# Performance work log

Hardware: AMD Instinct MI355X
Metric: run time of the kernel (lower is better)

The kernel has to match this reference:

```python
import jax, jax.numpy as jnp
import numpy as np

SCALE = 1.0

def setup_inputs() -> dict:
    key = jax.random.key(0)
    ks = jax.random.split(key, 7)
    B, S, I, O, R = 4, 4096, 1024, 1024, 256
    return {
        "x": jax.random.normal(ks[0], (B, S, I), dtype=jnp.float32),
        "base_weight": jax.random.normal(ks[1], (3 * O, I), dtype=jnp.float32) * 0.02,
        "base_bias": jax.random.normal(ks[2], (3 * O,), dtype=jnp.float32) * 0.02,
        "vera_A": jax.random.normal(ks[3], (R, I), dtype=jnp.float32) * 0.02,
        "vera_B": jax.random.normal(ks[4], (O, R), dtype=jnp.float32) * 0.02,
        "vera_d": jax.random.normal(ks[5], (2, R), dtype=jnp.float32) * 0.1,
        "vera_b": jax.random.normal(ks[6], (2, O), dtype=jnp.float32) * 0.1,
    }

def reference(x, base_weight, base_bias, vera_A, vera_B, vera_d, vera_b):
    # delta[k] = scale * diag(vera_b[k]) @ B @ diag(vera_d[k]) @ A  for k in {K, V}
    # implemented as (b[:,None]*B) @ (d[:,None]*A), batched over k via einsum
    O, I = vera_B.shape[0], vera_A.shape[1]
    deltas = SCALE * jnp.einsum("ko,or,kr,ri->koi", vera_b, vera_B, vera_d, vera_A)
    delta = deltas.reshape(2 * O, I)  # (2*O, I) stacked K,V deltas
    # kv_only=True: Q rows get zero delta, then K,V deltas
    zeros = jnp.zeros((base_weight.shape[0] - 2 * O, I), dtype=base_weight.dtype)
    full_delta = jnp.concatenate([zeros, delta], axis=0)  # (3*O, I)
    weight = base_weight + full_delta
    # linear: x @ weight.T + bias -> (B, S, 3*O)
    return jnp.einsum("bsi,oi->bso", x, weight) + base_bias
```

## Files before the change

### kernel.cpp

```cpp
#include <hip/hip_runtime.h>
#include <hip/hip_bf16.h>
#include <cstdint>
#include <cstddef>

typedef __bf16 bf16_t;
typedef __bf16 bf16x8 __attribute__((ext_vector_type(8)));
typedef __bf16 bf16x4 __attribute__((ext_vector_type(4)));
typedef float  f32x4  __attribute__((ext_vector_type(4)));

#define M_DIM 16384
#define N_DIM 3072
#define K_DIM 1024
#define R_DIM 256
#define O_DIM 1024

#define BM 128
#define BN 128
#define BK 32
#define NT_TILES 24
#define GRID_GEMM 3072
#define CHUNK_XCD 384

__device__ __forceinline__ void gload_lds16(const bf16_t* g, bf16_t* l) {
  __builtin_amdgcn_global_load_lds(
      (__attribute__((address_space(1))) void*)(g),
      (__attribute__((address_space(3))) void*)(l), 16, 0, 0);
}

__global__ __launch_bounds__(256) void prep_all(
    const float* __restrict__ x,
    const float* __restrict__ base_w,
    const float* __restrict__ vA,
    const float* __restrict__ vB,
    const float* __restrict__ vd,
    const float* __restrict__ vb,
    bf16_t* __restrict__ Wf,
    bf16_t* __restrict__ xh)
{
  const int blk = blockIdx.x;
  const int t = threadIdx.x;

  if (blk >= 384) {
    const size_t base = ((size_t)(blk - 384) * 256 + t) * 8;
    const f32x4 v0 = *(const f32x4*)(x + base);
    const f32x4 v1 = *(const f32x4*)(x + base + 4);
    bf16x8 o;
    o[0] = (bf16_t)v0[0]; o[1] = (bf16_t)v0[1]; o[2] = (bf16_t)v0[2]; o[3] = (bf16_t)v0[3];
    o[4] = (bf16_t)v1[0]; o[5] = (bf16_t)v1[1]; o[6] = (bf16_t)v1[2]; o[7] = (bf16_t)v1[3];
    *(bf16x8*)(xh + base) = o;
    return;
  }

  if (blk < 128) {
    const float* src = base_w + (size_t)blk * 8 * K_DIM;
    bf16_t*      dst = Wf + (size_t)blk * 8 * K_DIM;
#pragma unroll
    for (int rr = 0; rr < 8; ++rr) {
      const f32x4 v = *(const f32x4*)(src + rr * K_DIM + t * 4);
      bf16x4 ov;
      ov[0] = (bf16_t)v[0]; ov[1] = (bf16_t)v[1];
      ov[2] = (bf16_t)v[2]; ov[3] = (bf16_t)v[3];
      *(bf16x4*)(dst + rr * K_DIM + t * 4) = ov;
    }
    return;
  }

  const int rb = (blk - 128) * 8;
  const int k  = rb >> 10;
  const int ob = rb & 1023;

  __shared__ float coeffT[R_DIM][8];
  {
    const int r = t;
    const float d = vd[k * R_DIM + r];
#pragma unroll
    for (int rr = 0; rr < 8; ++rr) {
      const int o = ob + rr;
      coeffT[r][rr] = vb[k * O_DIM + o] * vB[(size_t)o * R_DIM + r] * d;
    }
  }
  __syncthreads();

  float acc[8][4];
#pragma unroll
  for (int rr = 0; rr < 8; ++rr)
#pragma unroll
    for (int c = 0; c < 4; ++c) acc[rr][c] = 0.0f;

  for (int r = 0; r < R_DIM; ++r) {
    const f32x4 av = *(const f32x4*)(vA + (size_t)r * K_DIM + t * 4);
    const f32x4 c0 = *(const f32x4*)&coeffT[r][0];
    const f32x4 c1 = *(const f32x4*)&coeffT[r][4];
#pragma unroll
    for (int rr = 0; rr < 8; ++rr) {
      const float cc = (rr < 4) ? c0[rr] : c1[rr - 4];
      acc[rr][0] += cc * av[0];
      acc[rr][1] += cc * av[1];
      acc[rr][2] += cc * av[2];
      acc[rr][3] += cc * av[3];
    }
  }

#pragma unroll
  for (int rr = 0; rr < 8; ++rr) {
    const size_t row = (size_t)(1024 + rb + rr);
    const f32x4 bw = *(const f32x4*)(base_w + row * K_DIM + t * 4);
    bf16x4 ov;
    ov[0] = (bf16_t)(bw[0] + acc[rr][0]);
    ov[1] = (bf16_t)(bw[1] + acc[rr][1]);
    ov[2] = (bf16_t)(bw[2] + acc[rr][2]);
    ov[3] = (bf16_t)(bw[3] + acc[rr][3]);
    *(bf16x4*)(Wf + row * K_DIM + t * 4) = ov;
  }
}

template <bool PRECONV>
__global__ __launch_bounds__(256) void gemm_qkv(
    const bf16_t* __restrict__ Xh,
    const float*  __restrict__ Xf,
    const bf16_t* __restrict__ W,
    const float*  __restrict__ bias,
    float* __restrict__ out)
{
  __shared__ bf16_t As[BM * BK];
  __shared__ bf16_t Bs[BN * BK];

  const int rawbid = blockIdx.x;
  const int bid = (rawbid & 7) * CHUNK_XCD + (rawbid >> 3);
  const int nt = bid % NT_TILES;
  const int mt = bid / NT_TILES;
  const int m0 = mt * BM;
  const int n0 = nt * BN;

  const int t = threadIdx.x;
  const int lane = t & 63;
  const int w = t >> 6;
  const int wm = w >> 1;
  const int wn = w & 1;

  const int r0 = t >> 2;
  const int c0 = (t & 3) * 8;

  const bf16_t* gB0 = W + (size_t)(n0 + r0) * K_DIM + c0;
  const bf16_t* gB1 = gB0 + (size_t)64 * K_DIM;
  bf16_t* lA0 = As + r0 * BK + c0;
  bf16_t* lA1 = As + (r0 + 64) * BK + c0;
  bf16_t* lB0 = Bs + r0 * BK + c0;
  bf16_t* lB1 = Bs + (r0 + 64) * BK + c0;

  const bf16_t* gA0h = nullptr; const bf16_t* gA1h = nullptr;
  const float*  gA0f = nullptr; const float*  gA1f = nullptr;
  if constexpr (PRECONV) {
    gA0h = Xh + (size_t)(m0 + r0) * K_DIM + c0;
    gA1h = gA0h + (size_t)64 * K_DIM;
  } else {
    gA0f = Xf + (size_t)(m0 + r0) * K_DIM + c0;
    gA1f = gA0f + (size_t)64 * K_DIM;
  }

  const f32x4 zero4 = {0.0f, 0.0f, 0.0f, 0.0f};
  f32x4 acc[4][4];
#pragma unroll
  for (int i = 0; i < 4; ++i)
#pragma unroll
    for (int j = 0; j < 4; ++j) acc[i][j] = zero4;

  const int row_a = wm * 64 + (lane & 15);
  const int row_b = wn * 64 + (lane & 15);
  const int kb = (lane >> 4) * 8;

  for (int k0 = 0; k0 < K_DIM; k0 += BK) {
    if constexpr (PRECONV) {
      gload_lds16(gA0h + k0, lA0);
      gload_lds16(gA1h + k0, lA1);
    } else {
      const f32x4 u0 = *(const f32x4*)(gA0f + k0);
      const f32x4 u1 = *(const f32x4*)(gA0f + k0 + 4);
      const f32x4 u2 = *(const f32x4*)(gA1f + k0);
      const f32x4 u3 = *(const f32x4*)(gA1f + k0 + 4);
      bf16x8 a0, a1;
#pragma unroll
      for (int c = 0; c < 4; ++c) {
        a0[c] = (bf16_t)u0[c]; a0[c + 4] = (bf16_t)u1[c];
        a1[c] = (bf16_t)u2[c]; a1[c + 4] = (bf16_t)u3[c];
      }
      *(bf16x8*)lA0 = a0;
      *(bf16x8*)lA1 = a1;
    }
    gload_lds16(gB0 + k0, lB0);
    gload_lds16(gB1 + k0, lB1);
    __syncthreads();

    bf16x8 a[4], b[4];
#pragma unroll
    for (int i = 0; i < 4; ++i)
      a[i] = *(const bf16x8*)(As + (row_a + i * 16) * BK + kb);
#pragma unroll
    for (int j = 0; j < 4; ++j)
      b[j] = *(const bf16x8*)(Bs + (row_b + j * 16) * BK + kb);

#pragma unroll
    for (int i = 0; i < 4; ++i)
#pragma unroll
      for (int j = 0; j < 4; ++j)
        acc[i][j] = __builtin_amdgcn_mfma_f32_16x16x32_bf16(a[i], b[j], acc[i][j], 0, 0, 0);

    __syncthreads();
  }

  const int colg = lane & 15;
  const int rq = (lane >> 4) * 4;
#pragma unroll
  for (int j = 0; j < 4; ++j) {
    const int n = n0 + wn * 64 + j * 16 + colg;
    const float bv = bias[n];
#pragma unroll
    for (int i = 0; i < 4; ++i) {
      const size_t mb = (size_t)(m0 + wm * 64 + i * 16 + rq);
#pragma unroll
      for (int r = 0; r < 4; ++r)
        out[(mb + r) * N_DIM + n] = acc[i][j][r] + bv;
    }
  }
}

extern "C" void kernel_launch(void* const* d_in, const int* in_sizes, int n_in,
                              void* d_out, int out_size, void* d_ws, size_t ws_size,
                              hipStream_t stream) {
  const float* x      = (const float*)d_in[0];
  const float* base_w = (const float*)d_in[1];
  const float* base_b = (const float*)d_in[2];
  const float* vA     = (const float*)d_in[3];
  const float* vB     = (const float*)d_in[4];
  const float* vd     = (const float*)d_in[5];
  const float* vb     = (const float*)d_in[6];
  float* out = (float*)d_out;

  const size_t xh_off   = 8u * 1024 * 1024;
  const size_t xh_bytes = (size_t)M_DIM * K_DIM * sizeof(bf16_t);

  bf16_t* Wf = (bf16_t*)d_ws;
  const bool preconv = ws_size >= xh_off + xh_bytes;
  bf16_t* Xh = preconv ? (bf16_t*)((char*)d_ws + xh_off) : nullptr;

  prep_all<<<preconv ? 8576 : 384, 256, 0, stream>>>(x, base_w, vA, vB, vd, vb, Wf, Xh);

  if (preconv)
    gemm_qkv<true><<<GRID_GEMM, 256, 0, stream>>>(Xh, nullptr, Wf, base_b, out);
  else
    gemm_qkv<false><<<GRID_GEMM, 256, 0, stream>>>(nullptr, x, Wf, base_b, out);
}
```

Measured before the change: 422.0 us.

## Add 256x256 double-buffered GEMM with swizzled LDS and interleaved prefetch

After: 412.0 us. 1.02x faster.

```diff
diff --git a/kernel.cpp b/kernel.cpp
--- a/kernel.cpp
+++ b/kernel.cpp
@@ -14,12 +14,15 @@
 #define R_DIM 256
 #define O_DIM 1024
 
-#define BM 128
-#define BN 128
-#define BK 32
-#define NT_TILES 24
-#define GRID_GEMM 3072
-#define CHUNK_XCD 384
+#define BM 256
+#define BN 256
+#define BK 64
+#define NTILE (N_DIM / BN)
+#define GRID_GEMM ((M_DIM / BM) * NTILE)
+#define CHUNK_XCD (GRID_GEMM / 8)
+#define SMEM_BYTES 131072
+
+#define REGN(c, isB, kh) ((c) * 32768 + (isB) * 16384 + (kh) * 8192)
 
 __device__ __forceinline__ void gload_lds16(const bf16_t* g, bf16_t* l) {
   __builtin_amdgcn_global_load_lds(
@@ -114,23 +117,169 @@
   }
 }
 
+__global__ __launch_bounds__(512, 2) void gemm_qkv(
+    const bf16_t* __restrict__ Xh,
+    const bf16_t* __restrict__ W,
+    const float*  __restrict__ bias,
+    float* __restrict__ out)
+{
+  extern __shared__ __align__(16) bf16_t sm[];
+
+  const int rawbid = blockIdx.x;
+  const int bid = (rawbid & 7) * CHUNK_XCD + (rawbid >> 3);
+  const int mt = bid / NTILE, nt = bid % NTILE;
+  const int m0 = mt * BM, n0 = nt * BN;
+
+  const int t = threadIdx.x;
+  const int lane = t & 63;
+  const int w = t >> 6;
+  const int wm = w >> 2;
+  const int wn = w & 3;
+
+  const int srow = t >> 2;
+  const int sig  = (t & 3) ^ ((t >> 3) & 3);
+  const bf16_t* pA0 = Xh + (size_t)(m0 + srow) * K_DIM + sig * 8;
+  const bf16_t* pA1 = pA0 + (size_t)128 * K_DIM;
+  const bf16_t* pB0 = W  + (size_t)(n0 + srow) * K_DIM + sig * 8;
+  const bf16_t* pB1 = pB0 + (size_t)128 * K_DIM;
+
+  const int rA = wm * 128 + (lane & 15);
+  const int rB = wn * 64  + (lane & 15);
+  const int aoff = rA * 32 + (((lane >> 4) ^ ((rA >> 1) & 3)) * 8);
+  const int boff = rB * 32 + (((lane >> 4) ^ ((rB >> 1) & 3)) * 8);
+
+  f32x4 acc[8][4];
+#pragma unroll
+  for (int i = 0; i < 8; ++i)
+#pragma unroll
+    for (int j = 0; j < 4; ++j) acc[i][j] = (f32x4){0.f, 0.f, 0.f, 0.f};
+
+#define STAGE(isB, c, kh, kb)                                              \
+  do {                                                                     \
+    const bf16_t* g0 = ((isB) ? pB0 : pA0) + (kb) + (kh) * 32;             \
+    const bf16_t* g1 = ((isB) ? pB1 : pA1) + (kb) + (kh) * 32;             \
+    bf16_t* l = sm + REGN(c, isB, kh) + w * 512;                           \
+    gload_lds16(g0, l);                                                    \
+    gload_lds16(g1, l + 4096);                                             \
+  } while (0)
+
+#define LOADA(c, kh)                                                       \
+  {                                                                        \
+    const bf16_t* base_ = sm + REGN(c, 0, kh) + aoff;                      \
+    _Pragma("unroll") for (int i = 0; i < 8; ++i)                          \
+        a[i] = *(const bf16x8*)(base_ + i * 512);                          \
+  }
+
+#define LOADB2(c, kh, j0)                                                  \
+  {                                                                        \
+    const bf16_t* base_ = sm + REGN(c, 1, kh) + boff;                      \
+    b[j0]     = *(const bf16x8*)(base_ + (j0) * 512);                      \
+    b[j0 + 1] = *(const bf16x8*)(base_ + ((j0) + 1) * 512);                \
+  }
+
+#define MFMA2(j0)                                                          \
+  __builtin_amdgcn_s_setprio(1);                                           \
+  _Pragma("unroll") for (int i = 0; i < 8; ++i) {                          \
+    acc[i][j0] = __builtin_amdgcn_mfma_f32_16x16x32_bf16(                  \
+        a[i], b[j0], acc[i][j0], 0, 0, 0);                                 \
+    acc[i][(j0) + 1] = __builtin_amdgcn_mfma_f32_16x16x32_bf16(            \
+        a[i], b[(j0) + 1], acc[i][(j0) + 1], 0, 0, 0);                     \
+  }                                                                        \
+  __builtin_amdgcn_s_setprio(0);
+
+#define WAITV(n) asm volatile("s_waitcnt vmcnt(" #n ")" ::: "memory")
+#define BARRIER()                                                          \
+  __builtin_amdgcn_s_barrier();                                            \
+  asm volatile("" ::: "memory")
+
+  bf16x8 a[8], b[4];
+
+  STAGE(0, 0, 0, 0);
+  STAGE(1, 0, 0, 0);
+  STAGE(0, 0, 1, 0);
+  STAGE(1, 0, 1, 0);
+
+  for (int tt = 0; tt < 15; ++tt) {
+    const int c = tt & 1, cn = c ^ 1;
+    const int kb = (tt + 1) * BK;
+    STAGE(0, cn, 0, kb);
+    WAITV(6);
+    BARRIER();
+    LOADA(c, 0);
+    LOADB2(c, 0, 0);
+    MFMA2(0);
+    STAGE(1, cn, 0, kb);
+    LOADB2(c, 0, 2);
+    MFMA2(2);
+    STAGE(0, cn, 1, kb);
+    WAITV(6);
+    BARRIER();
+    LOADA(c, 1);
+    LOADB2(c, 1, 0);
+    MFMA2(0);
+    STAGE(1, cn, 1, kb);
+    LOADB2(c, 1, 2);
+    MFMA2(2);
+  }
+
+  WAITV(4);
+  BARRIER();
+  LOADA(1, 0);
+  LOADB2(1, 0, 0);
+  MFMA2(0);
+  LOADB2(1, 0, 2);
+  MFMA2(2);
+  WAITV(0);
+  BARRIER();
+  LOADA(1, 1);
+  LOADB2(1, 1, 0);
+  MFMA2(0);
+  LOADB2(1, 1, 2);
+  MFMA2(2);
+
+  const int colg = lane & 15;
+  const int rq = (lane >> 4) * 4;
+#pragma unroll
+  for (int j = 0; j < 4; ++j) {
+    const int n = n0 + wn * 64 + j * 16 + colg;
+    const float bv = bias[n];
+#pragma unroll
+    for (int i = 0; i < 8; ++i) {
+      const size_t mb = (size_t)(m0 + wm * 128 + i * 16 + rq);
+#pragma unroll
+      for (int r = 0; r < 4; ++r)
+        out[(mb + r) * N_DIM + n] = acc[i][j][r] + bv;
+    }
+  }
+#undef STAGE
+#undef LOADA
+#undef LOADB2
+#undef MFMA2
+#undef WAITV
+#undef BARRIER
+}
+
+#define FBM 128
+#define FBN 128
+#define FBK 32
 template <bool PRECONV>
-__global__ __launch_bounds__(256) void gemm_qkv(
+__global__ __launch_bounds__(256) void gemm128(
     const bf16_t* __restrict__ Xh,
     const float*  __restrict__ Xf,
     const bf16_t* __restrict__ W,
     const float*  __restrict__ bias,
     float* __restrict__ out)
 {
-  __shared__ bf16_t As[BM * BK];
-  __shared__ bf16_t Bs[BN * BK];
+  __shared__ bf16_t As[FBM * FBK];
+  __shared__ bf16_t Bs[FBN * FBK];
 
   const int rawbid = blockIdx.x;
-  const int bid = (rawbid & 7) * CHUNK_XCD + (rawbid >> 3);
-  const int nt = bid % NT_TILES;
-  const int mt = bid / NT_TILES;
-  const int m0 = mt * BM;
-  const int n0 = nt * BN;
+  const int nblk = (M_DIM / FBM) * (N_DIM / FBN);
+  const int bid = (rawbid & 7) * (nblk / 8) + (rawbid >> 3);
+  const int nt = bid % (N_DIM / FBN);
+  const int mt = bid / (N_DIM / FBN);
+  const int m0 = mt * FBM;
+  const int n0 = nt * FBN;
 
   const int t = threadIdx.x;
   const int lane = t & 63;
@@ -143,10 +292,10 @@
 
   const bf16_t* gB0 = W + (size_t)(n0 + r0) * K_DIM + c0;
   const bf16_t* gB1 = gB0 + (size_t)64 * K_DIM;
-  bf16_t* lA0 = As + r0 * BK + c0;
-  bf16_t* lA1 = As + (r0 + 64) * BK + c0;
-  bf16_t* lB0 = Bs + r0 * BK + c0;
-  bf16_t* lB1 = Bs + (r0 + 64) * BK + c0;
+  bf16_t* lA0 = As + r0 * FBK + c0;
+  bf16_t* lA1 = As + (r0 + 64) * FBK + c0;
+  bf16_t* lB0 = Bs + r0 * FBK + c0;
+  bf16_t* lB1 = Bs + (r0 + 64) * FBK + c0;
 
   const bf16_t* gA0h = nullptr; const bf16_t* gA1h = nullptr;
   const float*  gA0f = nullptr; const float*  gA1f = nullptr;
@@ -158,18 +307,17 @@
     gA1f = gA0f + (size_t)64 * K_DIM;
   }
 
-  const f32x4 zero4 = {0.0f, 0.0f, 0.0f, 0.0f};
   f32x4 acc[4][4];
 #pragma unroll
   for (int i = 0; i < 4; ++i)
 #pragma unroll
-    for (int j = 0; j < 4; ++j) acc[i][j] = zero4;
+    for (int j = 0; j < 4; ++j) acc[i][j] = (f32x4){0.f, 0.f, 0.f, 0.f};
 
   const int row_a = wm * 64 + (lane & 15);
   const int row_b = wn * 64 + (lane & 15);
   const int kb = (lane >> 4) * 8;
 
-  for (int k0 = 0; k0 < K_DIM; k0 += BK) {
+  for (int k0 = 0; k0 < K_DIM; k0 += FBK) {
     if constexpr (PRECONV) {
       gload_lds16(gA0h + k0, lA0);
       gload_lds16(gA1h + k0, lA1);
@@ -194,10 +342,10 @@
     bf16x8 a[4], b[4];
 #pragma unroll
     for (int i = 0; i < 4; ++i)
-      a[i] = *(const bf16x8*)(As + (row_a + i * 16) * BK + kb);
+      a[i] = *(const bf16x8*)(As + (row_a + i * 16) * FBK + kb);
 #pragma unroll
     for (int j = 0; j < 4; ++j)
-      b[j] = *(const bf16x8*)(Bs + (row_b + j * 16) * BK + kb);
+      b[j] = *(const bf16x8*)(Bs + (row_b + j * 16) * FBK + kb);
 
 #pragma unroll
     for (int i = 0; i < 4; ++i)
@@ -243,10 +391,23 @@
   const bool preconv = ws_size >= xh_off + xh_bytes;
   bf16_t* Xh = preconv ? (bf16_t*)((char*)d_ws + xh_off) : nullptr;
 
+  static int smem_ok = -1;
+  if (smem_ok < 0) {
+    hipError_t e = hipFuncSetAttribute(
+        reinterpret_cast<const void*>(&gemm_qkv),
+        hipFuncAttributeMaxDynamicSharedMemorySize, SMEM_BYTES);
+    smem_ok = (e == hipSuccess) ? 1 : 0;
+  }
+
   prep_all<<<preconv ? 8576 : 384, 256, 0, stream>>>(x, base_w, vA, vB, vd, vb, Wf, Xh);
 
-  if (preconv)
-    gemm_qkv<true><<<GRID_GEMM, 256, 0, stream>>>(Xh, nullptr, Wf, base_b, out);
-  else
-    gemm_qkv<false><<<GRID_GEMM, 256, 0, stream>>>(nullptr, x, Wf, base_b, out);
+  if (preconv && smem_ok == 1) {
+    gemm_qkv<<<GRID_GEMM, 512, SMEM_BYTES, stream>>>(Xh, Wf, base_b, out);
+  } else if (preconv) {
+    gemm128<true><<<(M_DIM / FBM) * (N_DIM / FBN), 256, 0, stream>>>(
+        Xh, nullptr, Wf, base_b, out);
+  } else {
+    gemm128<false><<<(M_DIM / FBM) * (N_DIM / FBN), 256, 0, stream>>>(
+        nullptr, x, Wf, base_b, out);
+  }
 }
```
